# Kernel tuning notes

Measured on AMD Instinct MI355X. Metric: run time of the kernel, lower is better.

Reference implementation:

```python
import jax, jax.numpy as jnp
import numpy as np

WS = 7            # window_size
P = WS * WS       # tokens per window
NUM_HEADS = 12
N_SCALES = 3      # n_local_region_scales
LOCAL_HEAD = NUM_HEADS // N_SCALES

# relative position index (Swin-style), precomputed as a constant
_coords = np.stack(np.meshgrid(np.arange(WS), np.arange(WS), indexing='ij'))  # (2,WS,WS)
_cf = _coords.reshape(2, -1)                                                  # (2,P)
_rel = (_cf[:, :, None] - _cf[:, None, :]).transpose(1, 2, 0)                 # (P,P,2)
_rel[:, :, 0] += WS - 1
_rel[:, :, 1] += WS - 1
_rel[:, :, 0] *= 2 * WS - 1
REL_IDX = jnp.asarray(_rel.sum(-1))  # (P,P) int


def window_partition(arr, ws):
    # arr: (B, H, W, C) -> (B * H/ws * W/ws, ws, ws, C)
    B, H, W, C = arr.shape
    a = arr.reshape(B, H // ws, ws, W // ws, ws, C)
    return a.transpose(0, 1, 3, 2, 4, 5).reshape(-1, ws, ws, C)


def setup_inputs() -> dict:
    key = jax.random.key(0)
    ks = jax.random.split(key, 4)
    B, H, W, C = 16, 56, 56, 384
    N = H * W
    return {
        'x': jax.random.normal(ks[0], (B, N, C), dtype=jnp.float32),
        'w_qkv': jax.random.normal(ks[1], (C, 3 * C), dtype=jnp.float32) * 0.02,
        'w_proj': jax.random.normal(ks[2], (C, C), dtype=jnp.float32) * 0.02,
        'b_proj': jnp.zeros((C,), dtype=jnp.float32),
        'rel_bias_table': jax.random.normal(ks[3], ((2 * WS - 1) ** 2, LOCAL_HEAD), dtype=jnp.float32) * 0.02,
        'H': H,
        'W': W,
    }


def reference(x, w_qkv, w_proj, b_proj, rel_bias_table, H, W):
    B, N, C = x.shape
    head_dim = C // NUM_HEADS
    local_C = C // N_SCALES
    scale = head_dim ** -0.5

    # qkv projection (no bias), laid out as (3, B, N, C)
    temp = (x @ w_qkv).reshape(B, N, 3, C).transpose(2, 0, 1, 3)

    # relative position bias: (LOCAL_HEAD, P, P)
    bias = rel_bias_table[REL_IDX.reshape(-1)].reshape(P, P, LOCAL_HEAD).transpose(2, 0, 1)

    outs = []
    for i in range(N_SCALES):
        qkv = temp[:, :, :, i * local_C:(i + 1) * local_C]          # (3,B,N,local_C)
        oh, ow = H // (2 ** i), W // (2 ** i)
        n_region = (oh // WS) * (ow // WS)
        qkv = qkv.reshape(3 * B, N, local_C).transpose(0, 2, 1).reshape(3 * B, local_C, H, W)
        if i > 0:
            k = 2 ** i
            r = qkv.reshape(3 * B, local_C, oh, k, ow, k)
            qkv = r.mean(axis=(3, 5)) + r.max(axis=(3, 5))           # avg_pool + max_pool
        qkv = qkv.transpose(0, 2, 3, 1)                              # (3B, oh, ow, local_C)
        qkv = window_partition(qkv, WS)                              # (3B*n_region, WS, WS, local_C)
        qkv = qkv.reshape(3, B, n_region, WS, WS, LOCAL_HEAD, head_dim).transpose(0, 1, 5, 2, 3, 4, 6)
        # NOTE: the original reshapes (B,LOCAL_HEAD,n_region,WS,WS,hd) -> (-1,LOCAL_HEAD,P,hd),
        # which mixes batch/head/region axes; replicated faithfully (row-major reshape).
        q = qkv[0].reshape(-1, LOCAL_HEAD, P, head_dim)
        kk = qkv[1].reshape(-1, LOCAL_HEAD, P, head_dim)
        v = qkv[2].reshape(-1, LOCAL_HEAD, P, head_dim)
        attn = (q * scale) @ jnp.swapaxes(kk, -2, -1) + bias[None]   # (B*R, LH, P, P)
        attn = jax.nn.softmax(attn, axis=-1)
        y = attn @ v                                                 # (B*R, LH, P, hd)
        # faithful inverse of the mixed reshape + (non-inverse) window merge via plain reshape
        y = y.reshape(B, n_region, LOCAL_HEAD, P, head_dim).transpose(0, 2, 4, 1, 3)
        y = y.reshape(B, local_C, oh, ow)
        if i > 0:
            y = jax.image.resize(y, (B, local_C, H, W), method='bilinear')
        y = y.reshape(B, LOCAL_HEAD, head_dim, H, W).transpose(0, 1, 3, 4, 2)  # (B,LH,H,W,hd)
        outs.append(y)

    fused = jnp.concatenate(outs, axis=1)                            # (B,NUM_HEADS,H,W,hd)
    fused = fused.reshape(B, NUM_HEADS, N, C // NUM_HEADS).transpose(0, 2, 1, 3).reshape(B, N, C)
    return fused @ w_proj + b_proj
```

## Files before the change

### kernel.cpp

```cpp
#include <hip/hip_runtime.h>
#include <hip/hip_bf16.h>

typedef __hip_bfloat16 bf16;
typedef __hip_bfloat162 bf16x2;
typedef __attribute__((ext_vector_type(8))) short short8;
typedef __attribute__((ext_vector_type(4))) float f32x4;

__device__ __forceinline__ float bf2f(short v) {
  return __uint_as_float(((unsigned)(unsigned short)v) << 16);
}
__device__ __forceinline__ bf16 rawbf(short v) {
  unsigned short b = (unsigned short)v; return *(bf16*)&b;
}
__device__ __forceinline__ void storeOut(float* p, float v) { *p = v; }
__device__ __forceinline__ void storeOut(bf16* p, float v) { *p = __float2bfloat16(v); }

#define GLOAD_LDS16(g, l)                                              \
  __builtin_amdgcn_global_load_lds(                                    \
      (const __attribute__((address_space(1))) void*)(g),              \
      (__attribute__((address_space(3))) void*)(l), 16, 0, 0)

__global__ __launch_bounds__(256) void prep_kernel(const float* __restrict__ x,
                                                   const float* __restrict__ w_qkv,
                                                   const float* __restrict__ w_proj,
                                                   bf16* __restrict__ xb,
                                                   bf16* __restrict__ wqkvT,
                                                   bf16* __restrict__ wprojT)
{
  int bid = blockIdx.x;
  if (bid < 9408) {
    int i = bid * 256 + threadIdx.x;
    const float4* p = (const float4*)x + (size_t)i * 2;
    float4 a = p[0], b = p[1];
    union { short8 v; bf16 h[8]; } u;
    u.h[0] = __float2bfloat16(a.x); u.h[1] = __float2bfloat16(a.y);
    u.h[2] = __float2bfloat16(a.z); u.h[3] = __float2bfloat16(a.w);
    u.h[4] = __float2bfloat16(b.x); u.h[5] = __float2bfloat16(b.y);
    u.h[6] = __float2bfloat16(b.z); u.h[7] = __float2bfloat16(b.w);
    *((short8*)xb + i) = u.v;
  } else {
    int idx = (bid - 9408) * 256 + threadIdx.x;
    if (idx < 1152 * 384) {
      int n = idx / 384, k = idx - n * 384;
      wqkvT[idx] = __float2bfloat16(w_qkv[(size_t)k * 1152 + n]);
    } else {
      idx -= 1152 * 384;
      int n = idx / 384, k = idx - n * 384;
      wprojT[idx] = __float2bfloat16(w_proj[(size_t)k * 384 + n]);
    }
  }
}

template<typename TC, bool BIAS>
__global__ __launch_bounds__(512) void gemm_mfma(const bf16* __restrict__ A,
                                                 const bf16* __restrict__ Bt,
                                                 const float* __restrict__ bias,
                                                 TC* __restrict__ C,
                                                 int M, int N, int K, int nbx)
{
  __shared__ __align__(16) bf16 As[256 * 64];
  __shared__ __align__(16) bf16 Bs[128 * 64];
  const int tid = threadIdx.x;
  const int wave = tid >> 6, lane = tid & 63;
  const int nwg = gridDim.x;
  const int qc = nwg >> 3, rr = nwg & 7;
  const int xcd = blockIdx.x & 7, jj = blockIdx.x >> 3;
  const int wg = (xcd < rr ? xcd * (qc + 1) : rr * (qc + 1) + (xcd - rr) * qc) + jj;
  const int by = wg / nbx, bx = wg - by * nbx;
  const int bm = by * 256, bn = bx * 128;
  const int wr = wave >> 1, wc = wave & 1;

  f32x4 acc[4][4] = {};

  const bf16* aP[4];
  const bf16* bP[2];
#pragma unroll
  for (int e = 0; e < 4; ++e) {
    int flat = e * 8192 + tid * 16;
    int r = flat >> 7;
    int q = ((flat >> 4) & 7) ^ (r & 7);
    aP[e] = A + (size_t)(bm + r) * K + q * 8;
  }
#pragma unroll
  for (int e = 0; e < 2; ++e) {
    int flat = e * 8192 + tid * 16;
    int r = flat >> 7;
    int q = ((flat >> 4) & 7) ^ (r & 7);
    bP[e] = Bt + (size_t)(bn + r) * K + q * 8;
  }
  char* AsW = (char*)As + wave * 1024;
  char* BsW = (char*)Bs + wave * 1024;

  const int lr = lane & 15, lk = lane >> 4;
  const int rbA = (wr * 64 + lr) * 64;
  const int rbB = (wc * 64 + lr) * 64;
  const int q0 = ((lk    ) ^ (lr & 7)) * 8;
  const int q1 = ((4 + lk) ^ (lr & 7)) * 8;

  for (int k0 = 0; k0 < K; k0 += 64) {
#pragma unroll
    for (int e = 0; e < 4; ++e) GLOAD_LDS16(aP[e] + k0, AsW + e * 8192);
#pragma unroll
    for (int e = 0; e < 2; ++e) GLOAD_LDS16(bP[e] + k0, BsW + e * 8192);
    __syncthreads();
    short8 af0[4], af1[4], bf0[4], bf1[4];
#pragma unroll
    for (int i = 0; i < 4; ++i) {
      af0[i] = *(const short8*)(As + rbA + i * 1024 + q0);
      af1[i] = *(const short8*)(As + rbA + i * 1024 + q1);
    }
#pragma unroll
    for (int j = 0; j < 4; ++j) {
      bf0[j] = *(const short8*)(Bs + rbB + j * 1024 + q0);
      bf1[j] = *(const short8*)(Bs + rbB + j * 1024 + q1);
    }
#pragma unroll
    for (int i = 0; i < 4; ++i)
#pragma unroll
      for (int j = 0; j < 4; ++j) {
        acc[i][j] = __builtin_amdgcn_mfma_f32_16x16x32_bf16(af0[i], bf0[j], acc[i][j], 0, 0, 0);
        acc[i][j] = __builtin_amdgcn_mfma_f32_16x16x32_bf16(af1[i], bf1[j], acc[i][j], 0, 0, 0);
      }
    __syncthreads();
  }

  const int crow = bm + wr * 64 + lk * 4;
  const int ccol = bn + wc * 64 + lr;
#pragma unroll
  for (int j = 0; j < 4; ++j) {
    int col = ccol + j * 16;
    float bv = BIAS ? bias[col] : 0.f;
#pragma unroll
    for (int i = 0; i < 4; ++i)
#pragma unroll
      for (int t = 0; t < 4; ++t) {
        int row = crow + i * 16 + t;
        storeOut(&C[(size_t)row * N + col], acc[i][j][t] + bv);
      }
  }
}

struct AttnP {
  const bf16 *qb, *kb, *vb;
  bf16* out;
  int R, Rw, f, npos, out_cstride, out_coffset, blk0;
};

template<int F>
__device__ __forceinline__ void attn_body(const float* __restrict__ btable,
                                          const AttnP& p, int blk,
                                          bf16* KP, bf16* Vt, float* bias_s)
{
  const int b = blk / p.R, r = blk % p.R;
  const int rh = r / p.Rw, rw = r % p.Rw;
  const int tid = threadIdx.x;
  const int h = tid >> 6, lane = tid & 63;
  const int lr = lane & 15, lk = lane >> 4;
  const int hb = r & 3;
  const float pinv = 1.0f / (float)(F * F);

  if (tid < 169) bias_s[tid] = btable[tid * 4 + hb];

  const size_t gbase = (size_t)b * 3136 * 1152;

#pragma unroll
  for (int c0 = 0; c0 < 4; ++c0) {
    int j = c0 * 256 + tid;
    if (j < 784) {
      int row = j >> 4, r4 = j & 15;
      int hh = r4 >> 2, slot = r4 & 3;
      int r7 = (row * 9363) >> 16, rm = row - r7 * 7;
      const bf16* src = p.kb + gbase +
          ((size_t)((rh * 7 + r7) * F) * 56 + (rw * 7 + rm) * F) * 1152 + hh * 32 + slot * 8;
      short8 ov;
      if (F == 1) {
        ov = *(const short8*)src;
      } else {
        float sum[8] = {}, mx[8];
#pragma unroll
        for (int e = 0; e < 8; ++e) mx[e] = -3.4e38f;
#pragma unroll
        for (int dy = 0; dy < F; ++dy)
#pragma unroll
          for (int dx = 0; dx < F; ++dx) {
            short8 v = *(const short8*)(src + ((size_t)dy * 56 + dx) * 1152);
#pragma unroll
            for (int e = 0; e < 8; ++e) {
              float fv = bf2f(v[e]); sum[e] += fv; mx[e] = fmaxf(mx[e], fv);
            }
          }
        union { short8 v; bf16 hb8[8]; } u;
#pragma unroll
        for (int e = 0; e < 8; ++e) u.hb8[e] = __float2bfloat16(sum[e] * pinv + mx[e]);
        ov = u.v;
      }
      *(short8*)(KP + hh * 4096 + row * 40 + slot * 8) = ov;
    }
  }

#pragma unroll
  for (int c0 = 0; c0 < 4; ++c0) {
    int j = c0 * 256 + tid;
    int pp = j >> 4, r4 = j & 15;
    int hh = r4 >> 2, d8 = r4 & 3;
    bf16 hv[8];
    if (pp < 49) {
      int r7 = (pp * 9363) >> 16, rm = pp - r7 * 7;
      const bf16* src = p.vb + gbase +
          ((size_t)((rh * 7 + r7) * F) * 56 + (rw * 7 + rm) * F) * 1152 + hh * 32 + d8 * 8;
      if (F == 1) {
        short8 v = *(const short8*)src;
#pragma unroll
        for (int e = 0; e < 8; ++e) hv[e] = rawbf(v[e]);
      } else {
        float sum[8] = {}, mx[8];
#pragma unroll
        for (int e = 0; e < 8; ++e) mx[e] = -3.4e38f;
#pragma unroll
        for (int dy = 0; dy < F; ++dy)
#pragma unroll
          for (int dx = 0; dx < F; ++dx) {
            short8 v = *(const short8*)(src + ((size_t)dy * 56 + dx) * 1152);
#pragma unroll
            for (int e = 0; e < 8; ++e) {
              float fv = bf2f(v[e]); sum[e] += fv; mx[e] = fmaxf(mx[e], fv);
            }
          }
#pragma unroll
        for (int e = 0; e < 8; ++e) hv[e] = __float2bfloat16(sum[e] * pinv + mx[e]);
      }
    } else {
#pragma unroll
      for (int e = 0; e < 8; ++e) hv[e] = __float2bfloat16(0.f);
    }
#pragma unroll
    for (int e = 0; e < 8; ++e) {
      int d = d8 * 8 + e;
      Vt[hh * 2048 + d * 64 + ((pp >> 3) ^ (d & 7)) * 8 + (pp & 7)] = hv[e];
    }
  }

  short8 qa[4];
#pragma unroll
  for (int it = 0; it < 4; ++it) {
    int pq = it * 16 + lr; pq = min(pq, 48);
    int r7 = (pq * 9363) >> 16, rm = pq - r7 * 7;
    const bf16* src = p.qb + gbase +
        ((size_t)((rh * 7 + r7) * F) * 56 + (rw * 7 + rm) * F) * 1152 + h * 32 + lk * 8;
    if (F == 1) {
      qa[it] = *(const short8*)src;
    } else {
      float sum[8] = {}, mx[8];
#pragma unroll
      for (int e = 0; e < 8; ++e) mx[e] = -3.4e38f;
#pragma unroll
      for (int dy = 0; dy < F; ++dy)
#pragma unroll
        for (int dx = 0; dx < F; ++dx) {
          short8 v = *(const short8*)(src + ((size_t)dy * 56 + dx) * 1152);
#pragma unroll
          for (int e = 0; e < 8; ++e) {
            float fv = bf2f(v[e]); sum[e] += fv; mx[e] = fmaxf(mx[e], fv);
          }
        }
      union { short8 v; bf16 hb8[8]; } u;
#pragma unroll
      for (int e = 0; e < 8; ++e) u.hb8[e] = __float2bfloat16(sum[e] * pinv + mx[e]);
      qa[it] = u.v;
    }
  }

  __syncthreads();

  f32x4 s[4][4];
  {
    short8 kf[4];
#pragma unroll
    for (int jt = 0; jt < 4; ++jt)
      kf[jt] = *(const short8*)(KP + h * 4096 + (jt * 16 + lr) * 40 + lk * 8);
    const f32x4 z = {0.f, 0.f, 0.f, 0.f};
    __builtin_amdgcn_s_setprio(1);
#pragma unroll
    for (int it = 0; it < 4; ++it)
#pragma unroll
      for (int jt = 0; jt < 4; ++jt)
        s[it][jt] = __builtin_amdgcn_mfma_f32_16x16x32_bf16(qa[it], kf[jt], z, 0, 0, 0);
    __builtin_amdgcn_s_setprio(0);
  }

  const float scale = 0.17677669529663687f;
  const bool colpad = (lr != 0);
  int pp7[4], ppm[4];
#pragma unroll
  for (int jt = 0; jt < 4; ++jt) {
    int pp = min(jt * 16 + lr, 48);
    pp7[jt] = (pp * 9363) >> 16; ppm[jt] = pp - pp7[jt] * 7;
  }
  float sm[4][4];
#pragma unroll
  for (int it = 0; it < 4; ++it)
#pragma unroll
    for (int t = 0; t < 4; ++t) {
      int pq = min(it * 16 + lk * 4 + t, 48);
      int q7 = (pq * 9363) >> 16, qm = pq - q7 * 7;
#pragma unroll
      for (int jt = 0; jt < 4; ++jt) {
        float bv = bias_s[(q7 - pp7[jt] + 6) * 13 + (qm - ppm[jt] + 6)];
        float v = fmaf(s[it][jt][t], scale, bv);
        if (jt == 3 && colpad) v = -1e30f;
        s[it][jt][t] = v;
      }
      float m = fmaxf(fmaxf(s[it][0][t], s[it][1][t]), fmaxf(s[it][2][t], s[it][3][t]));
      m = fmaxf(m, __shfl_xor(m, 1));
      m = fmaxf(m, __shfl_xor(m, 2));
      m = fmaxf(m, __shfl_xor(m, 4));
      m = fmaxf(m, __shfl_xor(m, 8));
      float ssum = 0.f;
#pragma unroll
      for (int jt = 0; jt < 4; ++jt) {
        float e = __expf(s[it][jt][t] - m);
        s[it][jt][t] = e; ssum += e;
      }
      ssum += __shfl_xor(ssum, 1);
      ssum += __shfl_xor(ssum, 2);
      ssum += __shfl_xor(ssum, 4);
      ssum += __shfl_xor(ssum, 8);
      sm[it][t] = 1.0f / ssum;
    }

#pragma unroll
  for (int it = 0; it < 4; ++it)
#pragma unroll
    for (int t = 0; t < 4; ++t) {
      int prow = it * 16 + lk * 4 + t;
#pragma unroll
      for (int jt = 0; jt < 4; ++jt) {
        int slot = (jt * 2 + (lr >> 3)) ^ (prow & 7);
        KP[h * 4096 + prow * 64 + slot * 8 + (lr & 7)] = __float2bfloat16(s[it][jt][t]);
      }
    }
  __syncthreads();

  f32x4 o[4][2] = {};
#pragma unroll
  for (int ks = 0; ks < 2; ++ks) {
    short8 pf[4], vf[2];
#pragma unroll
    for (int it = 0; it < 4; ++it) {
      int prow = it * 16 + lr;
      pf[it] = *(const short8*)(KP + h * 4096 + prow * 64 + ((ks * 4 + lk) ^ (prow & 7)) * 8);
    }
#pragma unroll
    for (int jd = 0; jd < 2; ++jd) {
      int d = jd * 16 + lr;
      vf[jd] = *(const short8*)(Vt + h * 2048 + d * 64 + ((ks * 4 + lk) ^ (d & 7)) * 8);
    }
    __builtin_amdgcn_s_setprio(1);
#pragma unroll
    for (int it = 0; it < 4; ++it)
#pragma unroll
      for (int jd = 0; jd < 2; ++jd)
        o[it][jd] = __builtin_amdgcn_mfma_f32_16x16x32_bf16(pf[it], vf[jd], o[it][jd], 0, 0, 0);
    __builtin_amdgcn_s_setprio(0);
  }

  const int c0 = (r & 3) * 32;
#pragma unroll
  for (int it = 0; it < 4; ++it)
#pragma unroll
    for (int t = 0; t < 4; ++t) {
      int prow = it * 16 + lk * 4 + t;
      if (prow < 49) {
        int m_out = (h * (p.R >> 2) + (r >> 2)) * 49 + prow;
        bf16* op = p.out + ((size_t)b * p.npos + m_out) * p.out_cstride + p.out_coffset + c0;
#pragma unroll
        for (int jd = 0; jd < 2; ++jd)
          op[jd * 16 + lr] = __float2bfloat16(o[it][jd][t] * sm[it][t]);
      }
    }
}

__global__ __launch_bounds__(256) void attn_mfma(const float* __restrict__ btable,
                                                 AttnP P0, AttnP P1, AttnP P2)
{
  __shared__ __align__(16) bf16 KP[4 * 4096];
  __shared__ __align__(16) bf16 Vt[4 * 2048];
  __shared__ float bias_s[169];

  const AttnP p = (blockIdx.x >= (unsigned)P0.blk0) ? P0
                : (blockIdx.x >= (unsigned)P1.blk0) ? P1 : P2;
  const int blk = blockIdx.x - p.blk0;
  if (p.f == 1)      attn_body<1>(btable, p, blk, KP, Vt, bias_s);
  else if (p.f == 2) attn_body<2>(btable, p, blk, KP, Vt, bias_s);
  else               attn_body<4>(btable, p, blk, KP, Vt, bias_s);
}

__device__ __forceinline__ float2 bilerp2(const bf16* __restrict__ base, int dim, int h, int w, int cp)
{
  float r = (float)dim / 56.f;
  float uy = (h + 0.5f) * r - 0.5f;
  float ux = (w + 0.5f) * r - 0.5f;
  float fy0 = floorf(uy), fx0 = floorf(ux);
  int y0 = (int)fy0, x0 = (int)fx0;
  float fy = uy - fy0, fx = ux - fx0;
  int y0c = max(y0, 0), y1c = min(y0 + 1, dim - 1);
  int x0c = max(x0, 0), x1c = min(x0 + 1, dim - 1);
  bf16x2 v00 = *(const bf16x2*)(base + ((size_t)y0c * dim + x0c) * 128 + cp * 2);
  bf16x2 v01 = *(const bf16x2*)(base + ((size_t)y0c * dim + x1c) * 128 + cp * 2);
  bf16x2 v10 = *(const bf16x2*)(base + ((size_t)y1c * dim + x0c) * 128 + cp * 2);
  bf16x2 v11 = *(const bf16x2*)(base + ((size_t)y1c * dim + x1c) * 128 + cp * 2);
  float w00 = (1.f - fy) * (1.f - fx), w01 = (1.f - fy) * fx;
  float w10 = fy * (1.f - fx),        w11 = fy * fx;
  float2 o;
  o.x = w00 * __bfloat162float(v00.x) + w01 * __bfloat162float(v01.x) +
        w10 * __bfloat162float(v10.x) + w11 * __bfloat162float(v11.x);
  o.y = w00 * __bfloat162float(v00.y) + w01 * __bfloat162float(v01.y) +
        w10 * __bfloat162float(v10.y) + w11 * __bfloat162float(v11.y);
  return o;
}

__global__ __launch_bounds__(256) void upsample_both_kernel(const bf16* __restrict__ yb1,
                                                            const bf16* __restrict__ yb2,
                                                            bf16* __restrict__ fused)
{
  int t = blockIdx.x * 256 + threadIdx.x;
  int cp = t & 63;
  int pos = t >> 6;
  int n = pos % 3136, b = pos / 3136;
  int h = n / 56, w = n % 56;
  float2 s1 = bilerp2(yb1 + (size_t)b * 784 * 128, 28, h, w, cp);
  float2 s2 = bilerp2(yb2 + (size_t)b * 196 * 128, 14, h, w, cp);
  bf16* op = fused + (size_t)pos * 384;
  bf16x2 o1; o1.x = __float2bfloat16(s1.x); o1.y = __float2bfloat16(s1.y);
  bf16x2 o2; o2.x = __float2bfloat16(s2.x); o2.y = __float2bfloat16(s2.y);
  *(bf16x2*)(op + 128 + cp * 2) = o1;
  *(bf16x2*)(op + 256 + cp * 2) = o2;
}

extern "C" void kernel_launch(void* const* d_in, const int* in_sizes, int n_in,
                              void* d_out, int out_size, void* d_ws, size_t ws_size,
                              hipStream_t stream)
{
  const float* x      = (const float*)d_in[0];
  const float* w_qkv  = (const float*)d_in[1];
  const float* w_proj = (const float*)d_in[2];
  const float* b_proj = (const float*)d_in[3];
  const float* btable = (const float*)d_in[4];

  bf16* temp  = (bf16*)d_ws;
  bf16* fused = temp  + (size_t)50176 * 1152 + (size_t)3 * 16 * 980 * 128;
  bf16* ybuf1 = fused + (size_t)50176 * 384;
  bf16* ybuf2 = ybuf1 + (size_t)16 * 784 * 128;
  bf16* wqkvT = ybuf2 + (size_t)16 * 196 * 128;
  bf16* wprojT= wqkvT + (size_t)1152 * 384;
  bf16* xb    = fused;

  prep_kernel<<<9408 + 2304, 256, 0, stream>>>(x, w_qkv, w_proj, xb, wqkvT, wprojT);

  gemm_mfma<bf16, false><<<1764, 512, 0, stream>>>(
      xb, wqkvT, nullptr, temp, 50176, 1152, 384, 9);

  AttnP P2{temp + 256, temp + 640, temp + 1024, ybuf2,
           4, 2, 4, 196, 128, 0, 0};
  AttnP P1{temp + 128, temp + 512, temp + 896, ybuf1,
           16, 4, 2, 784, 128, 0, 64};
  AttnP P0{temp, temp + 384, temp + 768, fused,
           64, 8, 1, 3136, 384, 0, 320};
  attn_mfma<<<1344, 256, 0, stream>>>(btable, P0, P1, P2);

  upsample_both_kernel<<<16 * 3136 * 64 / 256, 256, 0, stream>>>(ybuf1, ybuf2, fused);

  gemm_mfma<float, true><<<588, 512, 0, stream>>>(
      fused, wprojT, b_proj, (float*)d_out, 50176, 384, 384, 3);
}
```

Before: 171.4 us.

## Double-buffer LDS tiles in MFMA GEMM to overlap global loads with compute

The GEMM kernel now keeps two LDS buffers for the A and B tiles and issues the global-to-LDS loads for the next K tile before computing on the current one. It uses explicit vmcnt waits and raw barriers in place of __syncthreads. The goal is to hide global memory latency behind the MFMA work. In exchange, LDS use doubles to 96KB per block, which may lower occupancy, and K is only 384, so there are just 6 iterations to overlap.

```diff
diff --git a/kernel.cpp b/kernel.cpp
--- a/kernel.cpp
+++ b/kernel.cpp
@@ -58,8 +58,8 @@
                                                  TC* __restrict__ C,
                                                  int M, int N, int K, int nbx)
 {
-  __shared__ __align__(16) bf16 As[256 * 64];
-  __shared__ __align__(16) bf16 Bs[128 * 64];
+  __shared__ __align__(16) bf16 As[2][256 * 64];
+  __shared__ __align__(16) bf16 Bs[2][128 * 64];
   const int tid = threadIdx.x;
   const int wave = tid >> 6, lane = tid & 63;
   const int nwg = gridDim.x;
@@ -88,8 +88,15 @@
     int q = ((flat >> 4) & 7) ^ (r & 7);
     bP[e] = Bt + (size_t)(bn + r) * K + q * 8;
   }
-  char* AsW = (char*)As + wave * 1024;
-  char* BsW = (char*)Bs + wave * 1024;
+
+  auto STAGE = [&](int buf, int k0) {
+    char* aw = (char*)(&As[buf][0]) + wave * 1024;
+    char* bw = (char*)(&Bs[buf][0]) + wave * 1024;
+#pragma unroll
+    for (int e = 0; e < 4; ++e) GLOAD_LDS16(aP[e] + k0, aw + e * 8192);
+#pragma unroll
+    for (int e = 0; e < 2; ++e) GLOAD_LDS16(bP[e] + k0, bw + e * 8192);
+  };
 
   const int lr = lane & 15, lk = lane >> 4;
   const int rbA = (wr * 64 + lr) * 64;
@@ -97,22 +104,29 @@
   const int q0 = ((lk    ) ^ (lr & 7)) * 8;
   const int q1 = ((4 + lk) ^ (lr & 7)) * 8;
 
-  for (int k0 = 0; k0 < K; k0 += 64) {
-#pragma unroll
-    for (int e = 0; e < 4; ++e) GLOAD_LDS16(aP[e] + k0, AsW + e * 8192);
-#pragma unroll
-    for (int e = 0; e < 2; ++e) GLOAD_LDS16(bP[e] + k0, BsW + e * 8192);
-    __syncthreads();
+  const int nt = K >> 6;
+  STAGE(0, 0);
+  int cur = 0;
+  for (int t = 0; t < nt; ++t) {
+    if (t + 1 < nt) {
+      STAGE(cur ^ 1, (t + 1) << 6);
+      asm volatile("s_waitcnt vmcnt(6)" ::: "memory");
+    } else {
+      asm volatile("s_waitcnt vmcnt(0)" ::: "memory");
+    }
+    __builtin_amdgcn_s_barrier();
+    const bf16* Ab = &As[cur][0];
+    const bf16* Bb = &Bs[cur][0];
     short8 af0[4], af1[4], bf0[4], bf1[4];
 #pragma unroll
     for (int i = 0; i < 4; ++i) {
-      af0[i] = *(const short8*)(As + rbA + i * 1024 + q0);
-      af1[i] = *(const short8*)(As + rbA + i * 1024 + q1);
+      af0[i] = *(const short8*)(Ab + rbA + i * 1024 + q0);
+      af1[i] = *(const short8*)(Ab + rbA + i * 1024 + q1);
     }
 #pragma unroll
     for (int j = 0; j < 4; ++j) {
-      bf0[j] = *(const short8*)(Bs + rbB + j * 1024 + q0);
-      bf1[j] = *(const short8*)(Bs + rbB + j * 1024 + q1);
+      bf0[j] = *(const short8*)(Bb + rbB + j * 1024 + q0);
+      bf1[j] = *(const short8*)(Bb + rbB + j * 1024 + q1);
     }
 #pragma unroll
     for (int i = 0; i < 4; ++i)
@@ -121,7 +135,9 @@
         acc[i][j] = __builtin_amdgcn_mfma_f32_16x16x32_bf16(af0[i], bf0[j], acc[i][j], 0, 0, 0);
         acc[i][j] = __builtin_amdgcn_mfma_f32_16x16x32_bf16(af1[i], bf1[j], acc[i][j], 0, 0, 0);
       }
-    __syncthreads();
+    asm volatile("s_waitcnt lgkmcnt(0)" ::: "memory");
+    __builtin_amdgcn_s_barrier();
+    cur ^= 1;
   }
 
   const int crow = bm + wr * 64 + lk * 4;
```

New measurement: 184.1 us. 7.4% more time.
